# Kernel optimization log

Hardware: AMD Instinct MI355X
Metric: run time of the kernel (lower is better)

The kernel has to match this reference:

```python
import jax, jax.numpy as jnp
import numpy as np
from functools import partial

H = 512
V = 32000


def setup_inputs() -> dict:
    key = jax.random.key(0)
    ks = jax.random.split(key, 16)
    B, Td, Te = 16, 64, 64
    s = 0.02
    inp = {
        'input_seqs': jax.random.normal(ks[0], (B, Td, H), jnp.float32),
        'input_lengths': jax.random.randint(ks[1], (B,), 1, Td + 1, jnp.int32),
        'encoder_outputs': jax.random.normal(ks[2], (B, Te, H), jnp.float32),
        'encoder_length': jax.random.randint(ks[3], (B,), 1, Te + 1, jnp.int32),
        # GRU (1 layer, batch_first): PyTorch layout W_ih (3H,H), W_hh (3H,H)
        'W_ih': jax.random.normal(ks[4], (3 * H, H), jnp.float32) * s,
        'W_hh': jax.random.normal(ks[5], (3 * H, H), jnp.float32) * s,
        'b_ih': jnp.zeros((3 * H,), jnp.float32),
        'b_hh': jnp.zeros((3 * H,), jnp.float32),
        # Attn: W: Linear(2H -> H), v: Linear(H -> 1)
        'W_attn': jax.random.normal(ks[6], (H, 2 * H), jnp.float32) * s,
        'b_attn': jnp.zeros((H,), jnp.float32),
        'v_w': jax.random.normal(ks[7], (H,), jnp.float32) * s,
        'v_b': jnp.zeros((), jnp.float32),
        # dense: Linear(2H -> H), output: Linear(H -> V)
        'W_dense': jax.random.normal(ks[8], (H, 2 * H), jnp.float32) * s,
        'b_dense': jnp.zeros((H,), jnp.float32),
        'W_out': jax.random.normal(ks[9], (V, H), jnp.float32) * s,
        'b_out': jnp.zeros((V,), jnp.float32),
    }
    return inp


def gru_forward(x, lengths, W_ih, W_hh, b_ih, b_hh):
    # Emulates pack_padded_sequence + GRU + pad_packed_sequence:
    # hidden state frozen past each sequence's length, outputs zero there.
    B, T, Hd = x.shape
    x_proj = jnp.einsum('bth,gh->btg', x, W_ih) + b_ih  # (B,T,3H)

    def step(h, inp):
        xp, t = inp  # xp: (B,3H)
        hp = h @ W_hh.T + b_hh
        xr, xz, xn = jnp.split(xp, 3, axis=-1)
        hr, hz, hn = jnp.split(hp, 3, axis=-1)
        r = jax.nn.sigmoid(xr + hr)
        z = jax.nn.sigmoid(xz + hz)
        n = jnp.tanh(xn + r * hn)
        h_new = (1.0 - z) * n + z * h
        valid = (t < lengths)[:, None]
        h_keep = jnp.where(valid, h_new, h)
        y = jnp.where(valid, h_new, 0.0)
        return h_keep, y

    h0 = jnp.zeros((B, Hd), x.dtype)
    h_last, ys = jax.lax.scan(step, h0, (x_proj.swapaxes(0, 1), jnp.arange(T)))
    return ys.swapaxes(0, 1), h_last  # (B,T,H), (B,H)


def attn_forward(enc, dec, enc_len, dec_len, W_attn, b_attn, v_w, v_b):
    B, Te, Hd = enc.shape
    Td = dec.shape[1]
    e_mask = (jnp.arange(Te) < enc_len[:, None])  # (B,Te)
    d_mask = (jnp.arange(Td) < dec_len[:, None])  # (B,Td)
    mask = (d_mask[:, :, None] & e_mask[:, None, :]).astype(enc.dtype)  # (B,Td,Te)
    # split W on the concat axis: cat(enc,dec) @ W.T = enc@We.T + dec@Wd.T
    We, Wd = W_attn[:, :Hd], W_attn[:, Hd:]
    enc_p = jnp.einsum('beh,gh->beg', enc, We)  # (B,Te,H)
    dec_p = jnp.einsum('bdh,gh->bdg', dec, Wd)  # (B,Td,H)
    m4 = mask[..., None]
    # masked-then-projected, matching enc_outputs*mask / dec_outputs*mask in torch
    score = jnp.tanh(enc_p[:, None, :, :] * m4 + dec_p[:, :, None, :] * m4 + b_attn)  # (B,Td,Te,H)
    energy = jnp.einsum('bdeh,h->bde', score, v_w) + v_b  # (B,Td,Te)
    a = jax.nn.softmax(energy, axis=2)  # softmax over ALL Te incl. masked (faithful)
    a_m = a * mask
    s = a_m.sum(axis=2)
    s = jnp.where(s == 0, 1.0, s)
    attention = a_m / s[:, :, None]  # (B,Td,Te)
    # attention is already zero where mask==0, so enc*mask == plain enc here
    context = jnp.einsum('bde,beh->bdh', attention, enc)
    return context  # dropout is identity at eval


def reference(input_seqs, input_lengths, encoder_outputs, encoder_length,
              W_ih, W_hh, b_ih, b_hh, W_attn, b_attn, v_w, v_b,
              W_dense, b_dense, W_out, b_out):
    dec_out, h_last = gru_forward(input_seqs, input_lengths, W_ih, W_hh, b_ih, b_hh)
    context = attn_forward(encoder_outputs, dec_out, encoder_length, input_lengths,
                           W_attn, b_attn, v_w, v_b)
    outputs = jnp.concatenate((dec_out, context), axis=2)  # (B,Td,2H)
    dense = jnp.tanh(jnp.einsum('bdg,hg->bdh', outputs, W_dense) + b_dense)
    logits = jnp.einsum('bdh,vh->bdv', dense, W_out) + b_out  # (B,Td,V)
    return logits, h_last[None]  # hidden: (n_layers=1, B, H)
```

## Files before the change

### kernel.cpp

```cpp
#include <hip/hip_runtime.h>
#include <stdint.h>


#define Hdim 512
#define Vdim 32000
#define Bdim 16
#define Tdim 64
#define BT   1024
#define GANG_BLOCKS 16

typedef __attribute__((ext_vector_type(8))) short bf16x8;
typedef __attribute__((ext_vector_type(4))) float f32x4;

static __device__ __forceinline__ unsigned short f2bf(float f) {
    unsigned u = __float_as_uint(f);
    u = u + 0x7FFFu + ((u >> 16) & 1u);
    return (unsigned short)(u >> 16);
}
static __device__ __forceinline__ float bf2f(unsigned short h) {
    return __uint_as_float((unsigned)h << 16);
}
static __device__ __forceinline__ float fast_tanh(float x) {
    return 2.f / (1.f + __expf(-2.f * x)) - 1.f;
}


#define U_ZERO 8320
#define U_INP  131072
#define U_WIH  196608
#define U_WAT  131072
#define U_WDE  131072
#define U_ENC  131072
#define U_SPLIT (U_INP + U_WIH + U_WAT + U_WDE + U_ENC)
#define U_WOUT 4096000
#define U_TOT  (U_ZERO + U_SPLIT + U_WOUT)

__global__ __launch_bounds__(256) void preproc_kernel(
    const float* __restrict__ input_seqs,
    const float* __restrict__ W_ih,
    const float* __restrict__ W_attn,
    const float* __restrict__ W_dense,
    const float* __restrict__ enc,
    const float* __restrict__ W_out,
    float* __restrict__ zero_base,
    unsigned short* __restrict__ inp_h, unsigned short* __restrict__ inp_l,
    unsigned short* __restrict__ Wih_h, unsigned short* __restrict__ Wih_l,
    unsigned short* __restrict__ Wat_h, unsigned short* __restrict__ Wat_l,
    unsigned short* __restrict__ Wde_h, unsigned short* __restrict__ Wde_l,
    unsigned short* __restrict__ enc_h, unsigned short* __restrict__ enc_l,
    unsigned short* __restrict__ Wout_bf)
{
    int u = blockIdx.x * 256 + threadIdx.x;
    const int stride = gridDim.x * 256;
    for (; u < U_TOT; u += stride) {
        int r = u;
        if (r < U_ZERO) {
            float4 z; z.x = 0.f; z.y = 0.f; z.z = 0.f; z.w = 0.f;
            *(float4*)(zero_base + r * 4) = z;
            continue;
        }
        r -= U_ZERO;
        if (r >= U_SPLIT) {
            int i = (r - U_SPLIT) * 4;
            float4 v = *(const float4*)(W_out + i);
            unsigned short h[4] = {f2bf(v.x), f2bf(v.y), f2bf(v.z), f2bf(v.w)};
            *(uint2*)(Wout_bf + i) = *(const uint2*)h;
            continue;
        }
        const float* src; unsigned short* hi; unsigned short* lo;
        if (r < U_INP) { src = input_seqs; hi = inp_h; lo = inp_l; }
        else { r -= U_INP;
            if (r < U_WIH) { src = W_ih; hi = Wih_h; lo = Wih_l; }
            else { r -= U_WIH;
                if (r < U_WAT) { src = W_attn; hi = Wat_h; lo = Wat_l; }
                else { r -= U_WAT;
                    if (r < U_WDE) { src = W_dense; hi = Wde_h; lo = Wde_l; }
                    else { r -= U_WDE; src = enc; hi = enc_h; lo = enc_l; }
                }
            }
        }
        int i = r * 4;
        float4 v = *(const float4*)(src + i);
        float f[4] = {v.x, v.y, v.z, v.w};
        unsigned short h[4], l[4];
#pragma unroll
        for (int k = 0; k < 4; ++k) {
            h[k] = f2bf(f[k]);
            l[k] = f2bf(f[k] - bf2f(h[k]));
        }
        *(uint2*)(hi + i) = *(const uint2*)h;
        *(uint2*)(lo + i) = *(const uint2*)l;
    }
}


struct GemmSmem {
    unsigned short AsH[128 * 40];
    unsigned short AsL[128 * 40];
    unsigned short BsH[128 * 40];
    unsigned short BsL[128 * 40];
};

static __device__ __forceinline__ void gemm_tile(
    GemmSmem& S, int m0, int n0,
    const unsigned short* __restrict__ Ah, const unsigned short* __restrict__ Al, int lda,
    const unsigned short* __restrict__ Bh, const unsigned short* __restrict__ Bl, int ldb,
    const float* __restrict__ bias,
    float* __restrict__ C, unsigned short* __restrict__ Cb, int ldc,
    int K, int act)
{
    const int tid = threadIdx.x;
    const int wave = tid >> 6, lane = tid & 63;
    const int wm = (wave >> 1) * 64, wn = (wave & 1) * 64;
    const int lrow = lane & 15, lk = (lane >> 4) * 8;

    f32x4 acc[4][4];
#pragma unroll
    for (int i = 0; i < 4; ++i)
#pragma unroll
        for (int j = 0; j < 4; ++j) acc[i][j] = (f32x4){0.f, 0.f, 0.f, 0.f};

    for (int k0 = 0; k0 < K; k0 += 32) {
#pragma unroll
        for (int i = 0; i < 2; ++i) {
            int idx = tid + i * 256;
            int rr = idx >> 2, kq = (idx & 3) * 8;
            size_t ao = (size_t)(m0 + rr) * lda + k0 + kq;
            size_t bo = (size_t)(n0 + rr) * ldb + k0 + kq;
            *(uint4*)(&S.AsH[rr * 40 + kq]) = *(const uint4*)(Ah + ao);
            *(uint4*)(&S.AsL[rr * 40 + kq]) = *(const uint4*)(Al + ao);
            *(uint4*)(&S.BsH[rr * 40 + kq]) = *(const uint4*)(Bh + bo);
            *(uint4*)(&S.BsL[rr * 40 + kq]) = *(const uint4*)(Bl + bo);
        }
        __syncthreads();
        bf16x8 ah[4], al[4], bh[4], bl[4];
#pragma unroll
        for (int i = 0; i < 4; ++i) {
            ah[i] = *(const bf16x8*)(&S.AsH[(wm + i * 16 + lrow) * 40 + lk]);
            al[i] = *(const bf16x8*)(&S.AsL[(wm + i * 16 + lrow) * 40 + lk]);
        }
#pragma unroll
        for (int j = 0; j < 4; ++j) {
            bh[j] = *(const bf16x8*)(&S.BsH[(wn + j * 16 + lrow) * 40 + lk]);
            bl[j] = *(const bf16x8*)(&S.BsL[(wn + j * 16 + lrow) * 40 + lk]);
        }
#pragma unroll
        for (int i = 0; i < 4; ++i)
#pragma unroll
            for (int j = 0; j < 4; ++j) {
                acc[i][j] = __builtin_amdgcn_mfma_f32_16x16x32_bf16(ah[i], bh[j], acc[i][j], 0, 0, 0);
                acc[i][j] = __builtin_amdgcn_mfma_f32_16x16x32_bf16(ah[i], bl[j], acc[i][j], 0, 0, 0);
                acc[i][j] = __builtin_amdgcn_mfma_f32_16x16x32_bf16(al[i], bh[j], acc[i][j], 0, 0, 0);
            }
        __syncthreads();
    }

    const int crow = m0 + wm + ((lane >> 4) * 4);
    const int ccol = n0 + wn + (lane & 15);
#pragma unroll
    for (int i = 0; i < 4; ++i) {
#pragma unroll
        for (int j = 0; j < 4; ++j) {
            int col = ccol + j * 16;
            float bv = bias[col];
#pragma unroll
            for (int rr = 0; rr < 4; ++rr) {
                int row = crow + i * 16 + rr;
                float v = acc[i][j][rr] + bv;
                if (act == 1) v = fast_tanh(v);
                if (Cb) Cb[(size_t)row * ldc + col] = f2bf(v);
                else    C [(size_t)row * ldc + col] = v;
            }
        }
    }
}

__global__ __launch_bounds__(256) void gemm_split(
    const unsigned short* __restrict__ Ah, const unsigned short* __restrict__ Al, int lda,
    const unsigned short* __restrict__ Bh, const unsigned short* __restrict__ Bl, int ldb,
    const float* __restrict__ bias,
    float* __restrict__ C, unsigned short* __restrict__ Cb, int ldc,
    int K, int act)
{
    __shared__ GemmSmem S;
    gemm_tile(S, blockIdx.y * 128, blockIdx.x * 128,
              Ah, Al, lda, Bh, Bl, ldb, bias, C, Cb, ldc, K, act);
}

__global__ __launch_bounds__(256) void gemm_split_dual(
    const unsigned short* __restrict__ A0h, const unsigned short* __restrict__ A0l,
    const unsigned short* __restrict__ B0h, const unsigned short* __restrict__ B0l,
    const float* __restrict__ bias0, float* __restrict__ C0,
    const unsigned short* __restrict__ A1h, const unsigned short* __restrict__ A1l,
    const unsigned short* __restrict__ B1h, const unsigned short* __restrict__ B1l,
    const float* __restrict__ bias1, float* __restrict__ C1)
{
    __shared__ GemmSmem S;
    const int bid = blockIdx.x;
    if (bid < 96) {
        gemm_tile(S, (bid / 12) * 128, (bid % 12) * 128,
                  A0h, A0l, Hdim, B0h, B0l, Hdim, bias0, C0, nullptr, 1536, Hdim, 0);
    } else {
        int r = bid - 96;
        gemm_tile(S, (r / 4) * 128, (r % 4) * 128,
                  A1h, A1l, Hdim, B1h, B1l, 1024, bias1, C1, nullptr, Hdim, Hdim, 0);
    }
}


__global__ __launch_bounds__(512) void gru_persistent(
    const float* __restrict__ xp,
    const float* __restrict__ Whh,
    const float* __restrict__ bhh,
    const int*   __restrict__ lengths,
    unsigned long long* __restrict__ hslots,
    unsigned short* __restrict__ cath,
    unsigned short* __restrict__ catl,
    float* __restrict__ h_last)
{
    const int bid  = blockIdx.x;
    const int b    = bid >> 4;
    const int blk  = bid & 15;
    const int tid  = threadIdx.x;
    const int wave = tid >> 6, lane = tid & 63;
    const int j0 = blk * 32 + wave * 4;
    const int k0 = lane * 8;

    __shared__ float hl[2][512];
    __shared__ unsigned short yh_buf[64][32];
    __shared__ unsigned short yl_buf[64][32];

    float w[12][8];
#pragma unroll
    for (int g = 0; g < 3; ++g)
#pragma unroll
        for (int jj = 0; jj < 4; ++jj) {
            const float* src = Whh + (size_t)(g * 512 + j0 + jj) * Hdim + k0;
            float4 a = *(const float4*)src;
            float4 bq = *(const float4*)(src + 4);
            int r = g * 4 + jj;
            w[r][0] = a.x;  w[r][1] = a.y;  w[r][2] = a.z;  w[r][3] = a.w;
            w[r][4] = bq.x; w[r][5] = bq.y; w[r][6] = bq.z; w[r][7] = bq.w;
        }

    const int j = j0 + (lane & 3);
    float bh_r = 0.f, bh_z = 0.f, bh_n = 0.f;
    if (lane < 4) {
        bh_r = bhh[j]; bh_z = bhh[512 + j]; bh_n = bhh[1024 + j];
    }
    const int len_b = lengths[b];
    float hprev = 0.f;

    const size_t PSTR = (size_t)Bdim * Hdim;
    unsigned long long* gslot = hslots + (size_t)b * Hdim;
    const float* xbase = xp + (size_t)b * Tdim * 1536;

    for (int t = 0; t < Tdim; ++t) {
        const int par = t & 1;

        float xr = 0.f, xz = 0.f, xn = 0.f;
        if (lane < 4) {
            const float* xrow = xbase + (size_t)t * 1536;
            xr = xrow[j]; xz = xrow[512 + j]; xn = xrow[1024 + j];
        }

        if (wave == 0) {
            const unsigned long long* sl = gslot + (size_t)par * PSTR + k0;
            unsigned long long v[8];
            bool ok;
            do {
#pragma unroll
                for (int q = 0; q < 8; ++q)
                    v[q] = __hip_atomic_load(sl + q, __ATOMIC_RELAXED,
                                             __HIP_MEMORY_SCOPE_AGENT);
                ok = true;
#pragma unroll
                for (int q = 0; q < 8; ++q)
                    ok = ok && ((unsigned)(v[q] >> 32) == (unsigned)t);
            } while (!ok);
#pragma unroll
            for (int q = 0; q < 8; ++q)
                hl[par][q * 64 + lane] = __uint_as_float((unsigned)v[q]);
        }
        __syncthreads();

        float hv[8];
#pragma unroll
        for (int q = 0; q < 8; ++q) hv[q] = hl[par][q * 64 + lane];

        float p[12];
#pragma unroll
        for (int r = 0; r < 12; ++r) {
            float s = 0.f;
#pragma unroll
            for (int k = 0; k < 8; ++k) s += w[r][k] * hv[k];
            p[r] = s;
        }

#pragma unroll
        for (int off = 1; off < 64; off <<= 1)
#pragma unroll
            for (int r = 0; r < 12; ++r)
                p[r] += __shfl_xor(p[r], off);

        if (lane < 4) {
            const int jj = lane;
            float hr = p[jj]     + bh_r;
            float hz = p[4 + jj] + bh_z;
            float hn = p[8 + jj] + bh_n;
            float rg = 1.f / (1.f + __expf(-(xr + hr)));
            float zg = 1.f / (1.f + __expf(-(xz + hz)));
            float ng = fast_tanh(xn + rg * hn);
            float hnew = (1.f - zg) * ng + zg * hprev;
            bool valid = t < len_b;
            float hkeep = valid ? hnew : hprev;
            hprev = hkeep;
            if (t < Tdim - 1) {
                unsigned long long pv =
                    ((unsigned long long)(unsigned)(t + 1) << 32) |
                    (unsigned long long)__float_as_uint(hkeep);
                __hip_atomic_store(gslot + (size_t)((t + 1) & 1) * PSTR + j, pv,
                                   __ATOMIC_RELAXED, __HIP_MEMORY_SCOPE_AGENT);
            } else {
                h_last[b * Hdim + j] = hkeep;
            }
            float y = valid ? hnew : 0.f;
            unsigned short yh = f2bf(y);
            yh_buf[t][wave * 4 + jj] = yh;
            yl_buf[t][wave * 4 + jj] = f2bf(y - bf2f(yh));
        }
    }

    __syncthreads();
    for (int idx = tid; idx < 64 * 16; idx += 512) {
        int t = idx >> 4, c = (idx & 15) * 2;
        size_t off = (size_t)(b * Tdim + t) * 1024 + blk * 32 + c;
        *(unsigned*)(cath + off) = *(const unsigned*)(&yh_buf[t][c]);
        *(unsigned*)(catl + off) = *(const unsigned*)(&yl_buf[t][c]);
    }
}


__global__ __launch_bounds__(256) void attn_kernel(
    const float* __restrict__ encp,
    const float* __restrict__ decp,
    const float* __restrict__ enc,
    const float* __restrict__ battn,
    const float* __restrict__ vw,
    const float* __restrict__ vb,
    const int* __restrict__ enc_len,
    const int* __restrict__ dec_len,
    unsigned short* __restrict__ cath,
    unsigned short* __restrict__ catl)
{
    const int blk = blockIdx.x;
    const int b = blk >> 6, d = blk & 63;
    const int tid = threadIdx.x;
    const size_t obase = (size_t)(b * Tdim + d) * 1024 + 512;

    if (d >= dec_len[b]) {
        for (int h = tid; h < Hdim; h += 256) { cath[obase + h] = 0; catl[obase + h] = 0; }
        return;
    }
    const int Tv = enc_len[b];

    __shared__ float part[64][4];
    __shared__ float a_lds[64];

    const int e = tid >> 2, p = tid & 3;
    float s = 0.f;
    if (e < Tv) {
        const float* ep = encp + (size_t)(b * Tdim + e) * Hdim;
        const float* dp = decp + (size_t)(b * Tdim + d) * Hdim;
        const int g0 = p * 128;
        for (int g = g0; g < g0 + 128; ++g)
            s += vw[g] * fast_tanh(ep[g] + dp[g] + battn[g]);
    }
    part[e][p] = s;
    __syncthreads();

    if (tid < 64) {
        const int e2 = tid;
        float en = (e2 < Tv) ? (part[e2][0] + part[e2][1] + part[e2][2] + part[e2][3] + vb[0]) : -1e30f;
        float m = en;
#pragma unroll
        for (int off = 32; off; off >>= 1) m = fmaxf(m, __shfl_xor(m, off));
        float ex = (e2 < Tv) ? __expf(en - m) : 0.f;
        float sum = ex;
#pragma unroll
        for (int off = 32; off; off >>= 1) sum += __shfl_xor(sum, off);
        a_lds[e2] = ex / sum;
    }
    __syncthreads();

    const int h = tid * 2;
    float c0 = 0.f, c1 = 0.f;
    for (int e3 = 0; e3 < Tv; ++e3) {
        float a = a_lds[e3];
        float2 ev = *(const float2*)(enc + (size_t)(b * Tdim + e3) * Hdim + h);
        c0 += a * ev.x; c1 += a * ev.y;
    }
    unsigned short h0 = f2bf(c0), h1 = f2bf(c1);
    cath[obase + h]     = h0;  catl[obase + h]     = f2bf(c0 - bf2f(h0));
    cath[obase + h + 1] = h1;  catl[obase + h + 1] = f2bf(c1 - bf2f(h1));
}


__global__ __launch_bounds__(512) void gemm_logits(
    const unsigned short* __restrict__ A,
    const unsigned short* __restrict__ B,
    const float* __restrict__ bias,
    float* __restrict__ C)
{
    const int K = Hdim;
    __shared__ unsigned short As[256 * 40];
    __shared__ unsigned short Bs[128 * 40];
    const int tid = threadIdx.x;
    const int m0 = blockIdx.y * 256, n0 = blockIdx.x * 128;
    const int wave = tid >> 6, lane = tid & 63;
    const int wm = (wave >> 1) * 64, wn = (wave & 1) * 64;
    const int lrow = lane & 15, lk = (lane >> 4) * 8;

    f32x4 acc[4][4];
#pragma unroll
    for (int i = 0; i < 4; ++i)
#pragma unroll
        for (int j = 0; j < 4; ++j) acc[i][j] = (f32x4){0.f, 0.f, 0.f, 0.f};

    for (int k0 = 0; k0 < K; k0 += 32) {
#pragma unroll
        for (int i = 0; i < 2; ++i) {
            int idx = tid + i * 512;
            int rr = idx >> 2, kq = (idx & 3) * 8;
            *(uint4*)(&As[rr * 40 + kq]) = *(const uint4*)(A + (size_t)(m0 + rr) * K + k0 + kq);
        }
        {
            int rr = tid >> 2, kq = (tid & 3) * 8;
            *(uint4*)(&Bs[rr * 40 + kq]) = *(const uint4*)(B + (size_t)(n0 + rr) * K + k0 + kq);
        }
        __syncthreads();
        bf16x8 af[4], bf[4];
#pragma unroll
        for (int i = 0; i < 4; ++i) af[i] = *(const bf16x8*)(&As[(wm + i * 16 + lrow) * 40 + lk]);
#pragma unroll
        for (int j = 0; j < 4; ++j) bf[j] = *(const bf16x8*)(&Bs[(wn + j * 16 + lrow) * 40 + lk]);
#pragma unroll
        for (int i = 0; i < 4; ++i)
#pragma unroll
            for (int j = 0; j < 4; ++j)
                acc[i][j] = __builtin_amdgcn_mfma_f32_16x16x32_bf16(af[i], bf[j], acc[i][j], 0, 0, 0);
        __syncthreads();
    }

    const int crow = m0 + wm + ((lane >> 4) * 4);
    const int ccol = n0 + wn + (lane & 15);
#pragma unroll
    for (int i = 0; i < 4; ++i) {
#pragma unroll
        for (int j = 0; j < 4; ++j) {
            int col = ccol + j * 16;
            float bv = bias[col];
#pragma unroll
            for (int rr = 0; rr < 4; ++rr) {
                int row = crow + i * 16 + rr;
                C[(size_t)row * Vdim + col] = acc[i][j][rr] + bv;
            }
        }
    }
}


extern "C" void kernel_launch(void* const* d_in, const int* in_sizes, int n_in,
                              void* d_out, int out_size, void* d_ws, size_t ws_size,
                              hipStream_t stream) {
    (void)in_sizes; (void)n_in; (void)out_size; (void)ws_size;

    const float* input_seqs  = (const float*)d_in[0];
    const int*   input_len   = (const int*)  d_in[1];
    const float* enc_out     = (const float*)d_in[2];
    const int*   enc_len     = (const int*)  d_in[3];
    const float* W_ih        = (const float*)d_in[4];
    const float* W_hh        = (const float*)d_in[5];
    const float* b_ih        = (const float*)d_in[6];
    const float* b_hh        = (const float*)d_in[7];
    const float* W_attn      = (const float*)d_in[8];
    const float* b_attn      = (const float*)d_in[9];
    const float* v_w         = (const float*)d_in[10];
    const float* v_b         = (const float*)d_in[11];
    const float* W_dense     = (const float*)d_in[12];
    const float* b_dense     = (const float*)d_in[13];
    const float* W_out       = (const float*)d_in[14];
    const float* b_out       = (const float*)d_in[15];

    float* logits = (float*)d_out;
    float* h_last = (float*)d_out + (size_t)BT * Vdim;

    float* ws    = (float*)d_ws;
    float* xp    = ws;
    float* encp  = xp   + 1572864;
    float* decp  = encp + 524288;
    unsigned long long* hslots = (unsigned long long*)(decp + 524288);
    float* zbias = (float*)(hslots + 16384);
    unsigned short* U0 = (unsigned short*)(zbias + 512);
    unsigned short* inp_h   = U0;
    unsigned short* inp_l   = U0 + 524288;
    unsigned short* Wih_h   = U0 + 1048576;
    unsigned short* Wih_l   = U0 + 1835008;
    unsigned short* Wattn_h = U0 + 2621440;
    unsigned short* Wattn_l = U0 + 3145728;
    unsigned short* Wden_h  = U0 + 3670016;
    unsigned short* Wden_l  = U0 + 4194304;
    unsigned short* enc_h   = U0 + 4718592;
    unsigned short* enc_l   = U0 + 5242880;
    unsigned short* Wout_bf = U0 + 5767168;
    unsigned short* cath = U0;
    unsigned short* catl = U0 + 1048576;
    unsigned short* dense_bf = (unsigned short*)encp;

    preproc_kernel<<<4096, 256, 0, stream>>>(
        input_seqs, W_ih, W_attn, W_dense, enc_out, W_out,
        (float*)hslots,
        inp_h, inp_l, Wih_h, Wih_l, Wattn_h, Wattn_l,
        Wden_h, Wden_l, enc_h, enc_l, Wout_bf);

    gemm_split_dual<<<128, 256, 0, stream>>>(
        inp_h, inp_l, Wih_h, Wih_l, b_ih, xp,
        enc_h, enc_l, Wattn_h, Wattn_l, zbias, encp);

    gru_persistent<<<Bdim * GANG_BLOCKS, 512, 0, stream>>>(
        xp, W_hh, b_hh, input_len, hslots, cath, catl, h_last);

    gemm_split<<<dim3(Hdim / 128, BT / 128), 256, 0, stream>>>(
        cath, catl, 1024, Wattn_h + 512, Wattn_l + 512, 1024, zbias, decp, nullptr, Hdim, Hdim, 0);

    attn_kernel<<<BT, 256, 0, stream>>>(encp, decp, enc_out, b_attn, v_w, v_b,
                                        enc_len, input_len, cath, catl);

    gemm_split<<<dim3(Hdim / 128, BT / 128), 256, 0, stream>>>(
        cath, catl, 1024, Wden_h, Wden_l, 1024, b_dense, nullptr, dense_bf, Hdim, 1024, 1);

    gemm_logits<<<dim3(Vdim / 128, BT / 256), 512, 0, stream>>>(
        dense_bf, Wout_bf, b_out, logits);
}
```

Before: 660.7 us.

## Overlap W_out bf16 conversion with GRU recurrence and vectorize attention scoring

Moves the large W_out fp32-to-bf16 conversion out of the preprocessing kernel and into extra blocks appended to the persistent GRU launch. Those blocks run beside the latency-bound recurrence instead of before it, so the conversion cost is meant to be hidden behind the serial GRU steps. The attention kernel also stages the decoder projection plus bias and v_w in shared memory and reads the encoder projection as float4. The risk is that the conversion blocks compete with the GRU gang blocks for CUs and memory bandwidth, and could delay their scheduling, which matters if the gang relies on co-residency for its spin synchronization.

```diff
diff --git a/kernel.cpp b/kernel.cpp
--- a/kernel.cpp
+++ b/kernel.cpp
@@ -8,6 +8,7 @@
 #define Tdim 64
 #define BT   1024
 #define GANG_BLOCKS 16
+#define CVT_BLOCKS 64
 
 typedef __attribute__((ext_vector_type(8))) short bf16x8;
 typedef __attribute__((ext_vector_type(4))) float f32x4;
@@ -32,8 +33,7 @@
 #define U_WDE  131072
 #define U_ENC  131072
 #define U_SPLIT (U_INP + U_WIH + U_WAT + U_WDE + U_ENC)
-#define U_WOUT 4096000
-#define U_TOT  (U_ZERO + U_SPLIT + U_WOUT)
+#define U_TOT  (U_ZERO + U_SPLIT)
 
 __global__ __launch_bounds__(256) void preproc_kernel(
     const float* __restrict__ input_seqs,
@@ -41,14 +41,12 @@
     const float* __restrict__ W_attn,
     const float* __restrict__ W_dense,
     const float* __restrict__ enc,
-    const float* __restrict__ W_out,
     float* __restrict__ zero_base,
     unsigned short* __restrict__ inp_h, unsigned short* __restrict__ inp_l,
     unsigned short* __restrict__ Wih_h, unsigned short* __restrict__ Wih_l,
     unsigned short* __restrict__ Wat_h, unsigned short* __restrict__ Wat_l,
     unsigned short* __restrict__ Wde_h, unsigned short* __restrict__ Wde_l,
-    unsigned short* __restrict__ enc_h, unsigned short* __restrict__ enc_l,
-    unsigned short* __restrict__ Wout_bf)
+    unsigned short* __restrict__ enc_h, unsigned short* __restrict__ enc_l)
 {
     int u = blockIdx.x * 256 + threadIdx.x;
     const int stride = gridDim.x * 256;
@@ -60,13 +58,6 @@
             continue;
         }
         r -= U_ZERO;
-        if (r >= U_SPLIT) {
-            int i = (r - U_SPLIT) * 4;
-            float4 v = *(const float4*)(W_out + i);
-            unsigned short h[4] = {f2bf(v.x), f2bf(v.y), f2bf(v.z), f2bf(v.w)};
-            *(uint2*)(Wout_bf + i) = *(const uint2*)h;
-            continue;
-        }
         const float* src; unsigned short* hi; unsigned short* lo;
         if (r < U_INP) { src = input_seqs; hi = inp_h; lo = inp_l; }
         else { r -= U_INP;
@@ -208,7 +199,7 @@
 }
 
 
-__global__ __launch_bounds__(512) void gru_persistent(
+__global__ __launch_bounds__(512) void gru_fused(
     const float* __restrict__ xp,
     const float* __restrict__ Whh,
     const float* __restrict__ bhh,
@@ -216,12 +207,26 @@
     unsigned long long* __restrict__ hslots,
     unsigned short* __restrict__ cath,
     unsigned short* __restrict__ catl,
-    float* __restrict__ h_last)
+    float* __restrict__ h_last,
+    const float* __restrict__ Wout_f,
+    unsigned short* __restrict__ Wout_bf)
 {
     const int bid  = blockIdx.x;
+    const int tid  = threadIdx.x;
+
+    if (bid >= Bdim * GANG_BLOCKS) {
+        int u = (bid - Bdim * GANG_BLOCKS) * 512 + tid;
+        const int STR = CVT_BLOCKS * 512;
+        for (; u < (Vdim * Hdim) / 4; u += STR) {
+            float4 v = *(const float4*)(Wout_f + (size_t)u * 4);
+            unsigned short h[4] = {f2bf(v.x), f2bf(v.y), f2bf(v.z), f2bf(v.w)};
+            *(uint2*)(Wout_bf + (size_t)u * 4) = *(const uint2*)h;
+        }
+        return;
+    }
+
     const int b    = bid >> 4;
     const int blk  = bid & 15;
-    const int tid  = threadIdx.x;
     const int wave = tid >> 6, lane = tid & 63;
     const int j0 = blk * 32 + wave * 4;
     const int k0 = lane * 8;
@@ -364,17 +369,34 @@
     }
     const int Tv = enc_len[b];
 
+    __shared__ float dpb[512];
+    __shared__ float vwl[512];
     __shared__ float part[64][4];
     __shared__ float a_lds[64];
+
+    if (tid < 128) {
+        const float4* dp4 = (const float4*)(decp + (size_t)(b * Tdim + d) * Hdim);
+        float4 dv = dp4[tid];
+        float4 bb = ((const float4*)battn)[tid];
+        float4 r; r.x = dv.x + bb.x; r.y = dv.y + bb.y;
+        r.z = dv.z + bb.z; r.w = dv.w + bb.w;
+        ((float4*)dpb)[tid] = r;
+        ((float4*)vwl)[tid] = ((const float4*)vw)[tid];
+    }
+    __syncthreads();
 
     const int e = tid >> 2, p = tid & 3;
     float s = 0.f;
     if (e < Tv) {
-        const float* ep = encp + (size_t)(b * Tdim + e) * Hdim;
-        const float* dp = decp + (size_t)(b * Tdim + d) * Hdim;
-        const int g0 = p * 128;
-        for (int g = g0; g < g0 + 128; ++g)
-            s += vw[g] * fast_tanh(ep[g] + dp[g] + battn[g]);
+        const float4* ep4 = (const float4*)(encp + (size_t)(b * Tdim + e) * Hdim);
+        const int q0 = p * 32;
+        for (int q = q0; q < q0 + 32; ++q) {
+            float4 ev = ep4[q];
+            s += vwl[q * 4 + 0] * fast_tanh(ev.x + dpb[q * 4 + 0]);
+            s += vwl[q * 4 + 1] * fast_tanh(ev.y + dpb[q * 4 + 1]);
+            s += vwl[q * 4 + 2] * fast_tanh(ev.z + dpb[q * 4 + 2]);
+            s += vwl[q * 4 + 3] * fast_tanh(ev.w + dpb[q * 4 + 3]);
+        }
     }
     part[e][p] = s;
     __syncthreads();
@@ -517,18 +539,19 @@
     unsigned short* catl = U0 + 1048576;
     unsigned short* dense_bf = (unsigned short*)encp;
 
-    preproc_kernel<<<4096, 256, 0, stream>>>(
-        input_seqs, W_ih, W_attn, W_dense, enc_out, W_out,
+    preproc_kernel<<<1024, 256, 0, stream>>>(
+        input_seqs, W_ih, W_attn, W_dense, enc_out,
         (float*)hslots,
         inp_h, inp_l, Wih_h, Wih_l, Wattn_h, Wattn_l,
-        Wden_h, Wden_l, enc_h, enc_l, Wout_bf);
+        Wden_h, Wden_l, enc_h, enc_l);
 
     gemm_split_dual<<<128, 256, 0, stream>>>(
         inp_h, inp_l, Wih_h, Wih_l, b_ih, xp,
         enc_h, enc_l, Wattn_h, Wattn_l, zbias, encp);
 
-    gru_persistent<<<Bdim * GANG_BLOCKS, 512, 0, stream>>>(
-        xp, W_hh, b_hh, input_len, hslots, cath, catl, h_last);
+    gru_fused<<<Bdim * GANG_BLOCKS + CVT_BLOCKS, 512, 0, stream>>>(
+        xp, W_hh, b_hh, input_len, hslots, cath, catl, h_last,
+        W_out, Wout_bf);
 
     gemm_split<<<dim3(Hdim / 128, BT / 128), 256, 0, stream>>>(
         cath, catl, 1024, Wattn_h + 512, Wattn_l + 512, 1024, zbias, decp, nullptr, Hdim, Hdim, 0);
```

Result: slower. 699.6 us (+5.9%).
